# Optimization experiments

Hardware: AMD Instinct MI355X
Metric: run time of the kernel (lower is better)

The kernel has to match this reference:

```python
import math
import jax, jax.numpy as jnp
import numpy as np

B, S, D, H = 2, 4096, 512, 8
DH = D // H


def setup_inputs() -> dict:
    key = jax.random.key(0)
    ks = jax.random.split(key, 12)
    lim = 1.0 / math.sqrt(D)
    u = lambda k, shp: jax.random.uniform(k, shp, jnp.float32, -lim, lim)
    return {
        "x": jax.random.normal(ks[0], (B, S, D), jnp.float32),
        "gamma": jax.random.uniform(ks[1], (B, S, 1), jnp.float32),
        "Wq": u(ks[2], (D, D)), "bq": u(ks[3], (D,)),
        "Wk": u(ks[4], (D, D)), "bk": u(ks[5], (D,)),
        "Wv": u(ks[6], (D, D)), "bv": u(ks[7], (D,)),
        "Wo": u(ks[8], (D, D)), "bo": u(ks[9], (D,)),
    }


def reference(x, gamma, Wq, bq, Wk, bk, Wv, bv, Wo, bo):
    b, s, d = x.shape
    # projections (torch Linear: x @ W.T + b), split heads -> [B,H,S,DH]
    def proj(W, bias):
        return (x @ W.T + bias).reshape(b, s, H, DH).transpose(0, 2, 1, 3)
    q, k, v = proj(Wq, bq), proj(Wk, bk), proj(Wv, bv)

    scores = jnp.einsum("bhsd,bhtd->bhst", q, k) / math.sqrt(DH)  # [B,H,S,S]
    causal = jnp.triu(jnp.ones((s, s), bool), k=1)  # True above diagonal
    neg_inf = jnp.float32(-jnp.inf)
    scores = jnp.where(causal[None, None], neg_inf, scores)

    # hyperbolic positional bias: -log1p(gamma_i * max(i-j, 0) + 1e-8)
    pos = jnp.arange(s)
    delta = jnp.clip(pos[:, None] - pos[None, :], 0).astype(jnp.float32)  # [S,S]
    gamma_q = gamma[:, :, 0][:, :, None]  # [B,S,1]
    hyper = -jnp.log1p(gamma_q * delta + 1e-8)  # [B,S,S]
    hyper = jnp.where(causal[None], neg_inf, hyper)
    scores = scores + hyper[:, None]  # [B,H,S,S]

    attn = jax.nn.softmax(scores, axis=-1)
    out = jnp.einsum("bhst,bhtd->bhsd", attn, v)  # [B,H,S,DH]
    out = out.transpose(0, 2, 1, 3).reshape(b, s, d)
    return out @ Wo.T + bo
```

## Files before the change

kernel.cpp:

```cpp
#include <hip/hip_runtime.h>
#include <hip/hip_bf16.h>

#define Bb 2
#define Ss 4096
#define Dd 512
#define Hh 8
#define DHh 64

typedef __attribute__((ext_vector_type(8))) short short8;
typedef __attribute__((ext_vector_type(4))) float floatx4;

static __device__ __forceinline__ ushort bfbits(float f) {
  union { __hip_bfloat16 h; ushort u; } cv;
  cv.h = __float2bfloat16(f);
  return cv.u;
}

static __device__ __forceinline__ unsigned int packhi(float a, float b) {
  union { float f; unsigned int u; } ca, cb; ca.f = a; cb.f = b;
  return (ca.u >> 16) | (cb.u & 0xffff0000u);
}

__global__ void cvt_all(const float* __restrict__ x,
                        const float* __restrict__ w0, const float* __restrict__ w1,
                        const float* __restrict__ w2, const float* __restrict__ w3,
                        ushort* __restrict__ out) {
  const int XN4 = (Bb * Ss * Dd) / 4;
  const int WN4 = (Dd * Dd) / 4;
  int i = blockIdx.x * blockDim.x + threadIdx.x;
  if (i >= XN4 + 4 * WN4) return;
  const float* s; int li;
  if (i < XN4) { s = x; li = i; }
  else {
    int t = i - XN4; int j = t >> 16; li = t & (WN4 - 1);
    s = (j == 0) ? w0 : (j == 1) ? w1 : (j == 2) ? w2 : w3;
  }
  float4 f = ((const float4*)s)[li];
  ushort4 u;
  u.x = bfbits(f.x); u.y = bfbits(f.y); u.z = bfbits(f.z); u.w = bfbits(f.w);
  ((ushort4*)out)[i] = u;
}

static __device__ __forceinline__ int vperm(int s0) {
  int kb = (s0 >> 4) & 3, gq = (s0 >> 2) & 3;
  return (s0 & ~63) | ((kb >> 1) << 5) | (gq << 3) | ((kb & 1) << 2);
}

#define LDQK(buf, k0)                                                          \
  _Pragma("unroll")                                                            \
  for (int rb = 0; rb < 4; ++rb)                                               \
    af[buf][rb] = *(const short8*)(ap + (size_t)rb * 16 * 512 + (k0));         \
  _Pragma("unroll")                                                            \
  for (int cb = 0; cb < 4; ++cb)                                               \
    bf[buf][cb] = *(const short8*)(bp + (size_t)cb * 16 * 512 + (k0));

__global__ __launch_bounds__(256) void qkv_gemm(
    const ushort* __restrict__ xb,
    const ushort* __restrict__ Wq, const ushort* __restrict__ Wk, const ushort* __restrict__ Wv,
    const float* __restrict__ bq, const float* __restrict__ bk, const float* __restrict__ bv,
    ushort* __restrict__ qo, ushort* __restrict__ ko, ushort* __restrict__ vo)
{
  int mb = blockIdx.x / 12, rest = blockIdx.x % 12;
  int which = rest >> 2, nb = rest & 3;
  const ushort* Bw  = (which == 0) ? Wq : (which == 1) ? Wk : Wv;
  const float* bias = (which == 0) ? bq : (which == 1) ? bk : bv;
  int lane = threadIdx.x & 63, w = threadIdx.x >> 6;
  int wr = w & 1, wc = w >> 1;
  int g = lane >> 4, ln = lane & 15;
  int m0 = mb * 128 + wr * 64;
  int c0 = nb * 128 + wc * 64;
  const ushort* ap = xb + (size_t)(m0 + ln) * 512 + g * 8;
  const ushort* bp = Bw + (size_t)(c0 + ln) * 512 + g * 8;
  floatx4 acc[4][4] = {};
  short8 af[2][4], bf[2][4];
  LDQK(0, 0)
#pragma unroll
  for (int it = 0; it < 16; ++it) {
    int cur = it & 1;
    if (it < 15) { LDQK(cur ^ 1, (it + 1) * 32) }
#pragma unroll
    for (int rb = 0; rb < 4; ++rb)
#pragma unroll
      for (int cb = 0; cb < 4; ++cb)
        acc[rb][cb] = __builtin_amdgcn_mfma_f32_16x16x32_bf16(af[cur][rb], bf[cur][cb], acc[rb][cb], 0, 0, 0);
  }
  float scale = (which == 0) ? 0.18033688011112042f : 1.0f;
#pragma unroll
  for (int rb = 0; rb < 4; ++rb)
#pragma unroll
    for (int cb = 0; cb < 4; ++cb) {
      int col = c0 + cb * 16 + ln;
      float bv_ = bias[col];
      int hh = col >> 6, dh = col & 63;
      if (which == 2) {
        int i0 = m0 + rb * 16 + g * 4;
        int bI = i0 >> 12, s0 = i0 & (Ss - 1);
        ushort4 pk;
        pk.x = bfbits(acc[rb][cb][0] + bv_);
        pk.y = bfbits(acc[rb][cb][1] + bv_);
        pk.z = bfbits(acc[rb][cb][2] + bv_);
        pk.w = bfbits(acc[rb][cb][3] + bv_);
        *(ushort4*)(vo + (((size_t)bI * Hh + hh) * DHh + dh) * Ss + vperm(s0)) = pk;
      } else {
        ushort* outp = (which == 0) ? qo : ko;
#pragma unroll
        for (int r = 0; r < 4; ++r) {
          int i = m0 + rb * 16 + g * 4 + r;
          int bI = i >> 12, s = i & (Ss - 1);
          outp[(((size_t)bI * Hh + hh) * Ss + s) * DHh + dh] = bfbits((acc[rb][cb][r] + bv_) * scale);
        }
      }
    }
}

#define LD32(buf, k0)                                                          \
  af[buf][0] = *(const short8*)(ap + (k0));                                    \
  af[buf][1] = *(const short8*)(ap + 16 * 512 + (k0));                         \
  _Pragma("unroll")                                                            \
  for (int ns = 0; ns < 4; ++ns)                                               \
    bfr[buf][ns] = *(const short8*)(bp + (size_t)ns * 16 * 512 + (k0));

__global__ __launch_bounds__(256) void gemm_out(
    const ushort* __restrict__ A, const ushort* __restrict__ Bw,
    const float* __restrict__ bias, float* __restrict__ outp)
{
  int mb = blockIdx.x >> 3, nb = blockIdx.x & 7;
  int lane = threadIdx.x & 63, w = threadIdx.x >> 6;
  int g = lane >> 4, ln = lane & 15;
  int m0 = mb * 128 + w * 32;
  const ushort* ap = A + (size_t)(m0 + ln) * 512 + g * 8;
  const ushort* bp = Bw + (size_t)(nb * 64 + ln) * 512 + g * 8;
  floatx4 acc[2][4] = {};
  short8 af[2][2], bfr[2][4];
  LD32(0, 0)
#pragma unroll
  for (int it = 0; it < 16; ++it) {
    int cur = it & 1;
    if (it < 15) { LD32(cur ^ 1, (it + 1) * 32) }
#pragma unroll
    for (int ns = 0; ns < 4; ++ns) {
      acc[0][ns] = __builtin_amdgcn_mfma_f32_16x16x32_bf16(af[cur][0], bfr[cur][ns], acc[0][ns], 0, 0, 0);
      acc[1][ns] = __builtin_amdgcn_mfma_f32_16x16x32_bf16(af[cur][1], bfr[cur][ns], acc[1][ns], 0, 0, 0);
    }
  }
#pragma unroll
  for (int rb = 0; rb < 2; ++rb)
#pragma unroll
    for (int ns = 0; ns < 4; ++ns) {
      int col = nb * 64 + ns * 16 + ln;
      float bv_ = bias[col];
#pragma unroll
      for (int r = 0; r < 4; ++r)
        outp[(size_t)(m0 + rb * 16 + g * 4 + r) * 512 + col] = acc[rb][ns][r] + bv_;
    }
}

__global__ __launch_bounds__(128) void flash8(
    const ushort* __restrict__ q, const ushort* __restrict__ k,
    const ushort* __restrict__ vt, const float* __restrict__ gamma,
    ushort* __restrict__ o)
{
  __shared__ __align__(16) float Pmrg[64][34];
  __shared__ __align__(16) ushort Tb[16 * 72];

  int z = blockIdx.x;
  int bh = z & 15;
  int b = bh >> 3, hh = bh & 7;
  int sslot = (z >> 4) & 15, rnd = z >> 8;
  int j = (rnd << 4) | ((rnd & 1) ? (15 - sslot) : sslot);
  int u = j >> 1, qsel = j & 1;

  int tid = threadIdx.x;
  int half = tid >> 6, lane = tid & 63;
  int g = lane >> 4, ln = lane & 15;

  const ushort* kp = k + ((size_t)bh * Ss + ln) * DHh + g * 8;
  const ushort* vp = vt + ((size_t)bh * DHh + ln) * Ss + g * 8;

  int t = 2 * u + qsel;
  int q0 = t * 32;
  int ktm = u;
  int nkt = u + 1;
  int h = nkt >> 1;
  int lo = half ? h : 0, hi = half ? nkt : h;

  const ushort* qp = q + ((size_t)bh * Ss + q0 + ln) * DHh + g * 8;
  short8 qf00 = *(const short8*)qp;
  short8 qf01 = *(const short8*)(qp + 32);
  short8 qf10 = *(const short8*)(qp + 16 * DHh);
  short8 qf11 = *(const short8*)(qp + 16 * DHh + 32);

  int qrow0 = q0 + ln, qrow1 = q0 + 16 + ln;
  float gm0 = gamma[(size_t)b * Ss + qrow0];
  float gm1 = gamma[(size_t)b * Ss + qrow1];
  float l2[2] = {0.0f, 0.0f};
  floatx4 oacc[2][4] = {};

  short8 kfl[4], kfh[4], vf[8];
  int kb0 = lo * 64;
#pragma unroll
  for (int ns = 0; ns < 4; ++ns) {
    kfl[ns] = *(const short8*)(kp + (size_t)(kb0 + ns * 16) * DHh);
    kfh[ns] = *(const short8*)(kp + (size_t)(kb0 + ns * 16) * DHh + 32);
  }
#pragma unroll
  for (int cc = 0; cc < 8; ++cc)
    vf[cc] = *(const short8*)(vp + (size_t)((cc & 3) * 16) * Ss + kb0 + (cc >> 2) * 32);

  for (int kt = lo; kt < hi; ++kt) {
    int kbase = kt * 64;
    float sv[2][16];
#pragma unroll
    for (int ns = 0; ns < 4; ++ns) {
      floatx4 z0 = {}, z1 = {};
      z0 = __builtin_amdgcn_mfma_f32_16x16x32_bf16(kfl[ns], qf00, z0, 0, 0, 0);
      z0 = __builtin_amdgcn_mfma_f32_16x16x32_bf16(kfh[ns], qf01, z0, 0, 0, 0);
      z1 = __builtin_amdgcn_mfma_f32_16x16x32_bf16(kfl[ns], qf10, z1, 0, 0, 0);
      z1 = __builtin_amdgcn_mfma_f32_16x16x32_bf16(kfh[ns], qf11, z1, 0, 0, 0);
#pragma unroll
      for (int r = 0; r < 4; ++r) { sv[0][ns * 4 + r] = z0[r]; sv[1][ns * 4 + r] = z1[r]; }
    }
    if (kt + 1 < hi) {
      const ushort* kn = kp + (size_t)(kbase + 64) * DHh;
#pragma unroll
      for (int ns = 0; ns < 4; ++ns) {
        kfl[ns] = *(const short8*)(kn + (size_t)(ns * 16) * DHh);
        kfh[ns] = *(const short8*)(kn + (size_t)(ns * 16) * DHh + 32);
      }
    }
    bool last = (kt == ktm);
    short8 pfrag[2][2];
#pragma unroll
    for (int qb = 0; qb < 2; ++qb) {
      int qrow = qb ? qrow1 : qrow0;
      float gm = qb ? gm1 : gm0;
      int db = qrow - kbase - g * 4;
      float fd = (float)db;
      float rsub[4] = {0.0f, 0.0f, 0.0f, 0.0f};
      if (last) {
#pragma unroll
        for (int e = 0; e < 16; ++e) {
          int off = (e >> 2) * 16 + (e & 3);
          if (db - off < 0) sv[qb][e] = -1e30f;
          float delta = fmaxf(fd - (float)off, 0.0f);
          float wt = __builtin_amdgcn_rcpf(fmaf(gm, delta, 1.0f));
          float pv = __builtin_amdgcn_exp2f(sv[qb][e]) * wt;
          rsub[e & 3] += pv;
          sv[qb][e] = pv;
        }
      } else {
#pragma unroll
        for (int e = 0; e < 16; ++e) {
          float delta = fd - (float)((e >> 2) * 16 + (e & 3));
          float wt = __builtin_amdgcn_rcpf(fmaf(gm, delta, 1.0f));
          float pv = __builtin_amdgcn_exp2f(sv[qb][e]) * wt;
          rsub[e & 3] += pv;
          sv[qb][e] = pv;
        }
      }
      l2[qb] += (rsub[0] + rsub[1]) + (rsub[2] + rsub[3]);
#pragma unroll
      for (int c = 0; c < 2; ++c) {
        uint4 pkd;
        pkd.x = packhi(sv[qb][8 * c + 0], sv[qb][8 * c + 1]);
        pkd.y = packhi(sv[qb][8 * c + 2], sv[qb][8 * c + 3]);
        pkd.z = packhi(sv[qb][8 * c + 4], sv[qb][8 * c + 5]);
        pkd.w = packhi(sv[qb][8 * c + 6], sv[qb][8 * c + 7]);
        pfrag[qb][c] = *(short8*)&pkd;
      }
    }
#pragma unroll
    for (int c = 0; c < 2; ++c)
#pragma unroll
      for (int ds = 0; ds < 4; ++ds) {
        oacc[0][ds] = __builtin_amdgcn_mfma_f32_16x16x32_bf16(vf[c * 4 + ds], pfrag[0][c], oacc[0][ds], 0, 0, 0);
        oacc[1][ds] = __builtin_amdgcn_mfma_f32_16x16x32_bf16(vf[c * 4 + ds], pfrag[1][c], oacc[1][ds], 0, 0, 0);
      }
    if (kt + 1 < hi) {
#pragma unroll
      for (int cc = 0; cc < 8; ++cc)
        vf[cc] = *(const short8*)(vp + (size_t)((cc & 3) * 16) * Ss + kbase + 64 + (cc >> 2) * 32);
    }
  }

  if (half) {
#pragma unroll
    for (int qb = 0; qb < 2; ++qb)
#pragma unroll
      for (int ds = 0; ds < 4; ++ds)
#pragma unroll
        for (int r = 0; r < 4; ++r)
          Pmrg[lane][qb * 16 + ds * 4 + r] = oacc[qb][ds][r];
    Pmrg[lane][32] = l2[0];
    Pmrg[lane][33] = l2[1];
  }
  __syncthreads();
  if (!half) {
#pragma unroll
    for (int qb = 0; qb < 2; ++qb) {
#pragma unroll
      for (int ds = 0; ds < 4; ++ds)
#pragma unroll
        for (int r = 0; r < 4; ++r)
          oacc[qb][ds][r] += Pmrg[lane][qb * 16 + ds * 4 + r];
      float l = l2[qb] + Pmrg[lane][32 + qb];
      l += __shfl_xor(l, 16);
      l += __shfl_xor(l, 32);
      float linv = 1.0f / l;
      ushort* tb = &Tb[0];
#pragma unroll
      for (int ds = 0; ds < 4; ++ds)
#pragma unroll
        for (int r = 0; r < 4; ++r)
          tb[ln * 72 + ds * 16 + g * 4 + r] = bfbits(oacc[qb][ds][r] * linv);
      short8 v0 = *(const short8*)(tb + ln * 72 + g * 16);
      short8 v1 = *(const short8*)(tb + ln * 72 + g * 16 + 8);
      size_t oa = ((size_t)b * Ss + q0 + qb * 16 + ln) * Dd + hh * DHh + g * 16;
      *(short8*)(o + oa) = v0;
      *(short8*)(o + oa + 8) = v1;
    }
  }
}

extern "C" void kernel_launch(void* const* d_in, const int* in_sizes, int n_in,
                              void* d_out, int out_size, void* d_ws, size_t ws_size,
                              hipStream_t stream) {
  const float* x     = (const float*)d_in[0];
  const float* gamma = (const float*)d_in[1];
  const float* Wq    = (const float*)d_in[2];
  const float* bq    = (const float*)d_in[3];
  const float* Wk    = (const float*)d_in[4];
  const float* bk    = (const float*)d_in[5];
  const float* Wv    = (const float*)d_in[6];
  const float* bv    = (const float*)d_in[7];
  const float* Wo    = (const float*)d_in[8];
  const float* bo    = (const float*)d_in[9];

  const size_t NX = (size_t)Bb * Ss * Dd;
  const size_t NW = (size_t)Dd * Dd;
  ushort* xb  = (ushort*)d_ws;
  ushort* Wqb = xb + NX;
  ushort* Wkb = Wqb + NW;
  ushort* Wvb = Wkb + NW;
  ushort* Wob = Wvb + NW;
  ushort* qb  = Wob + NW;
  ushort* kb  = qb + NX;
  ushort* vtb = kb + NX;
  ushort* ab  = vtb + NX;

  const int total4 = (int)(NX / 4 + 4 * (NW / 4));
  cvt_all<<<(total4 + 255) / 256, 256, 0, stream>>>(x, Wq, Wk, Wv, Wo, xb);

  qkv_gemm<<<64 * 12, 256, 0, stream>>>(xb, Wqb, Wkb, Wvb, bq, bk, bv, qb, kb, vtb);

  flash8<<<2048, 128, 0, stream>>>(qb, kb, vtb, gamma, ab);

  gemm_out<<<512, 256, 0, stream>>>(ab, Wob, bo, (float*)d_out);
}
```

Baseline: 292.6 us.

## Pair complementary causal query tiles per block and split KV range over four waves

Replaces the 2-wave flash kernel with a 4-wave block that handles two query tiles, p and 63-p, so every block does the same total number of KV tiles. The 65 KV tiles are split evenly across the four waves, and partial outputs and row sums are combined with LDS atomicAdd into per-tile accumulators. This removes the load imbalance of the causal triangle and halves the grid. The cost is LDS atomic traffic, zero-initialisation of the accumulators, and an extra Q/gamma reload when a wave crosses the boundary between the two tiles.

New measurement: 305.6 us. +4.4%, slower.

```diff
diff --git a/kernel.cpp b/kernel.cpp
--- a/kernel.cpp
+++ b/kernel.cpp
@@ -155,164 +155,174 @@
     }
 }
 
-__global__ __launch_bounds__(128) void flash8(
+__global__ __launch_bounds__(256) void flash9(
     const ushort* __restrict__ q, const ushort* __restrict__ k,
     const ushort* __restrict__ vt, const float* __restrict__ gamma,
     ushort* __restrict__ o)
 {
-  __shared__ __align__(16) float Pmrg[64][34];
-  __shared__ __align__(16) ushort Tb[16 * 72];
+  __shared__ __align__(16) float Pacc[2][64][34];
+  __shared__ __align__(16) ushort Tb[2][16 * 72];
 
   int z = blockIdx.x;
   int bh = z & 15;
   int b = bh >> 3, hh = bh & 7;
-  int sslot = (z >> 4) & 15, rnd = z >> 8;
-  int j = (rnd << 4) | ((rnd & 1) ? (15 - sslot) : sslot);
-  int u = j >> 1, qsel = j & 1;
+  int qsel = (z >> 4) & 1;
+  int p = z >> 5;
+  int c = p + 1;
 
   int tid = threadIdx.x;
-  int half = tid >> 6, lane = tid & 63;
+  int wv = tid >> 6, lane = tid & 63;
   int g = lane >> 4, ln = lane & 15;
+
+  {
+    float* pz = &Pacc[0][0][0];
+#pragma unroll
+    for (int i = 0; i < 17; ++i) pz[tid + 256 * i] = 0.0f;
+  }
+  __syncthreads();
 
   const ushort* kp = k + ((size_t)bh * Ss + ln) * DHh + g * 8;
   const ushort* vp = vt + ((size_t)bh * DHh + ln) * Ss + g * 8;
 
-  int t = 2 * u + qsel;
-  int q0 = t * 32;
-  int ktm = u;
-  int nkt = u + 1;
-  int h = nkt >> 1;
-  int lo = half ? h : 0, hi = half ? nkt : h;
-
-  const ushort* qp = q + ((size_t)bh * Ss + q0 + ln) * DHh + g * 8;
-  short8 qf00 = *(const short8*)qp;
-  short8 qf01 = *(const short8*)(qp + 32);
-  short8 qf10 = *(const short8*)(qp + 16 * DHh);
-  short8 qf11 = *(const short8*)(qp + 16 * DHh + 32);
-
-  int qrow0 = q0 + ln, qrow1 = q0 + 16 + ln;
-  float gm0 = gamma[(size_t)b * Ss + qrow0];
-  float gm1 = gamma[(size_t)b * Ss + qrow1];
-  float l2[2] = {0.0f, 0.0f};
-  floatx4 oacc[2][4] = {};
-
-  short8 kfl[4], kfh[4], vf[8];
-  int kb0 = lo * 64;
-#pragma unroll
-  for (int ns = 0; ns < 4; ++ns) {
-    kfl[ns] = *(const short8*)(kp + (size_t)(kb0 + ns * 16) * DHh);
-    kfh[ns] = *(const short8*)(kp + (size_t)(kb0 + ns * 16) * DHh + 32);
-  }
-#pragma unroll
-  for (int cc = 0; cc < 8; ++cc)
-    vf[cc] = *(const short8*)(vp + (size_t)((cc & 3) * 16) * Ss + kb0 + (cc >> 2) * 32);
-
-  for (int kt = lo; kt < hi; ++kt) {
-    int kbase = kt * 64;
-    float sv[2][16];
+  int bw = 16 * wv + (wv > 0 ? 1 : 0);
+  int ew = 16 * (wv + 1) + 1;
+
+  for (int seg = 0; seg < 2; ++seg) {
+    int lo, hi, ut;
+    if (seg == 0) { lo = bw; hi = min(ew, c); ut = p; }
+    else { int s = max(bw, c); lo = s - c; hi = ew - c; ut = 63 - p; }
+    if (lo >= hi) continue;
+
+    int t = 2 * ut + qsel;
+    int q0 = t * 32;
+    int ktm = ut;
+
+    const ushort* qp = q + ((size_t)bh * Ss + q0 + ln) * DHh + g * 8;
+    short8 qf00 = *(const short8*)qp;
+    short8 qf01 = *(const short8*)(qp + 32);
+    short8 qf10 = *(const short8*)(qp + 16 * DHh);
+    short8 qf11 = *(const short8*)(qp + 16 * DHh + 32);
+
+    int qrow0 = q0 + ln, qrow1 = q0 + 16 + ln;
+    float gm0 = gamma[(size_t)b * Ss + qrow0];
+    float gm1 = gamma[(size_t)b * Ss + qrow1];
+    float l2[2] = {0.0f, 0.0f};
+    floatx4 oacc[2][4] = {};
+
+    short8 kfl[4], kfh[4], vf[8];
+    int kb0 = lo * 64;
 #pragma unroll
     for (int ns = 0; ns < 4; ++ns) {
-      floatx4 z0 = {}, z1 = {};
-      z0 = __builtin_amdgcn_mfma_f32_16x16x32_bf16(kfl[ns], qf00, z0, 0, 0, 0);
-      z0 = __builtin_amdgcn_mfma_f32_16x16x32_bf16(kfh[ns], qf01, z0, 0, 0, 0);
-      z1 = __builtin_amdgcn_mfma_f32_16x16x32_bf16(kfl[ns], qf10, z1, 0, 0, 0);
-      z1 = __builtin_amdgcn_mfma_f32_16x16x32_bf16(kfh[ns], qf11, z1, 0, 0, 0);
-#pragma unroll
-      for (int r = 0; r < 4; ++r) { sv[0][ns * 4 + r] = z0[r]; sv[1][ns * 4 + r] = z1[r]; }
-    }
-    if (kt + 1 < hi) {
-      const ushort* kn = kp + (size_t)(kbase + 64) * DHh;
+      kfl[ns] = *(const short8*)(kp + (size_t)(kb0 + ns * 16) * DHh);
+      kfh[ns] = *(const short8*)(kp + (size_t)(kb0 + ns * 16) * DHh + 32);
+    }
+#pragma unroll
+    for (int cc = 0; cc < 8; ++cc)
+      vf[cc] = *(const short8*)(vp + (size_t)((cc & 3) * 16) * Ss + kb0 + (cc >> 2) * 32);
+
+    for (int kt = lo; kt < hi; ++kt) {
+      int kbase = kt * 64;
+      float sv[2][16];
 #pragma unroll
       for (int ns = 0; ns < 4; ++ns) {
-        kfl[ns] = *(const short8*)(kn + (size_t)(ns * 16) * DHh);
-        kfh[ns] = *(const short8*)(kn + (size_t)(ns * 16) * DHh + 32);
-      }
-    }
-    bool last = (kt == ktm);
-    short8 pfrag[2][2];
+        floatx4 z0 = {}, z1 = {};
+        z0 = __builtin_amdgcn_mfma_f32_16x16x32_bf16(kfl[ns], qf00, z0, 0, 0, 0);
+        z0 = __builtin_amdgcn_mfma_f32_16x16x32_bf16(kfh[ns], qf01, z0, 0, 0, 0);
+        z1 = __builtin_amdgcn_mfma_f32_16x16x32_bf16(kfl[ns], qf10, z1, 0, 0, 0);
+        z1 = __builtin_amdgcn_mfma_f32_16x16x32_bf16(kfh[ns], qf11, z1, 0, 0, 0);
+#pragma unroll
+        for (int r = 0; r < 4; ++r) { sv[0][ns * 4 + r] = z0[r]; sv[1][ns * 4 + r] = z1[r]; }
+      }
+      if (kt + 1 < hi) {
+        const ushort* kn = kp + (size_t)(kbase + 64) * DHh;
+#pragma unroll
+        for (int ns = 0; ns < 4; ++ns) {
+          kfl[ns] = *(const short8*)(kn + (size_t)(ns * 16) * DHh);
+          kfh[ns] = *(const short8*)(kn + (size_t)(ns * 16) * DHh + 32);
+        }
+      }
+      bool last = (kt == ktm);
+      short8 pfrag[2][2];
+#pragma unroll
+      for (int qb = 0; qb < 2; ++qb) {
+        int qrow = qb ? qrow1 : qrow0;
+        float gm = qb ? gm1 : gm0;
+        int db = qrow - kbase - g * 4;
+        float fd = (float)db;
+        float rsub[4] = {0.0f, 0.0f, 0.0f, 0.0f};
+        if (last) {
+#pragma unroll
+          for (int e = 0; e < 16; ++e) {
+            int off = (e >> 2) * 16 + (e & 3);
+            if (db - off < 0) sv[qb][e] = -1e30f;
+            float delta = fmaxf(fd - (float)off, 0.0f);
+            float wt = __builtin_amdgcn_rcpf(fmaf(gm, delta, 1.0f));
+            float pv = __builtin_amdgcn_exp2f(sv[qb][e]) * wt;
+            rsub[e & 3] += pv;
+            sv[qb][e] = pv;
+          }
+        } else {
+#pragma unroll
+          for (int e = 0; e < 16; ++e) {
+            float delta = fd - (float)((e >> 2) * 16 + (e & 3));
+            float wt = __builtin_amdgcn_rcpf(fmaf(gm, delta, 1.0f));
+            float pv = __builtin_amdgcn_exp2f(sv[qb][e]) * wt;
+            rsub[e & 3] += pv;
+            sv[qb][e] = pv;
+          }
+        }
+        l2[qb] += (rsub[0] + rsub[1]) + (rsub[2] + rsub[3]);
+#pragma unroll
+        for (int cc = 0; cc < 2; ++cc) {
+          uint4 pkd;
+          pkd.x = packhi(sv[qb][8 * cc + 0], sv[qb][8 * cc + 1]);
+          pkd.y = packhi(sv[qb][8 * cc + 2], sv[qb][8 * cc + 3]);
+          pkd.z = packhi(sv[qb][8 * cc + 4], sv[qb][8 * cc + 5]);
+          pkd.w = packhi(sv[qb][8 * cc + 6], sv[qb][8 * cc + 7]);
+          pfrag[qb][cc] = *(short8*)&pkd;
+        }
+      }
+#pragma unroll
+      for (int cc = 0; cc < 2; ++cc)
+#pragma unroll
+        for (int ds = 0; ds < 4; ++ds) {
+          oacc[0][ds] = __builtin_amdgcn_mfma_f32_16x16x32_bf16(vf[cc * 4 + ds], pfrag[0][cc], oacc[0][ds], 0, 0, 0);
+          oacc[1][ds] = __builtin_amdgcn_mfma_f32_16x16x32_bf16(vf[cc * 4 + ds], pfrag[1][cc], oacc[1][ds], 0, 0, 0);
+        }
+      if (kt + 1 < hi) {
+#pragma unroll
+        for (int cc = 0; cc < 8; ++cc)
+          vf[cc] = *(const short8*)(vp + (size_t)((cc & 3) * 16) * Ss + kbase + 64 + (cc >> 2) * 32);
+      }
+    }
+
 #pragma unroll
     for (int qb = 0; qb < 2; ++qb) {
-      int qrow = qb ? qrow1 : qrow0;
-      float gm = qb ? gm1 : gm0;
-      int db = qrow - kbase - g * 4;
-      float fd = (float)db;
-      float rsub[4] = {0.0f, 0.0f, 0.0f, 0.0f};
-      if (last) {
-#pragma unroll
-        for (int e = 0; e < 16; ++e) {
-          int off = (e >> 2) * 16 + (e & 3);
-          if (db - off < 0) sv[qb][e] = -1e30f;
-          float delta = fmaxf(fd - (float)off, 0.0f);
-          float wt = __builtin_amdgcn_rcpf(fmaf(gm, delta, 1.0f));
-          float pv = __builtin_amdgcn_exp2f(sv[qb][e]) * wt;
-          rsub[e & 3] += pv;
-          sv[qb][e] = pv;
-        }
-      } else {
-#pragma unroll
-        for (int e = 0; e < 16; ++e) {
-          float delta = fd - (float)((e >> 2) * 16 + (e & 3));
-          float wt = __builtin_amdgcn_rcpf(fmaf(gm, delta, 1.0f));
-          float pv = __builtin_amdgcn_exp2f(sv[qb][e]) * wt;
-          rsub[e & 3] += pv;
-          sv[qb][e] = pv;
-        }
-      }
-      l2[qb] += (rsub[0] + rsub[1]) + (rsub[2] + rsub[3]);
-#pragma unroll
-      for (int c = 0; c < 2; ++c) {
-        uint4 pkd;
-        pkd.x = packhi(sv[qb][8 * c + 0], sv[qb][8 * c + 1]);
-        pkd.y = packhi(sv[qb][8 * c + 2], sv[qb][8 * c + 3]);
-        pkd.z = packhi(sv[qb][8 * c + 4], sv[qb][8 * c + 5]);
-        pkd.w = packhi(sv[qb][8 * c + 6], sv[qb][8 * c + 7]);
-        pfrag[qb][c] = *(short8*)&pkd;
-      }
-    }
-#pragma unroll
-    for (int c = 0; c < 2; ++c)
-#pragma unroll
-      for (int ds = 0; ds < 4; ++ds) {
-        oacc[0][ds] = __builtin_amdgcn_mfma_f32_16x16x32_bf16(vf[c * 4 + ds], pfrag[0][c], oacc[0][ds], 0, 0, 0);
-        oacc[1][ds] = __builtin_amdgcn_mfma_f32_16x16x32_bf16(vf[c * 4 + ds], pfrag[1][c], oacc[1][ds], 0, 0, 0);
-      }
-    if (kt + 1 < hi) {
-#pragma unroll
-      for (int cc = 0; cc < 8; ++cc)
-        vf[cc] = *(const short8*)(vp + (size_t)((cc & 3) * 16) * Ss + kbase + 64 + (cc >> 2) * 32);
-    }
-  }
-
-  if (half) {
-#pragma unroll
-    for (int qb = 0; qb < 2; ++qb)
 #pragma unroll
       for (int ds = 0; ds < 4; ++ds)
 #pragma unroll
         for (int r = 0; r < 4; ++r)
-          Pmrg[lane][qb * 16 + ds * 4 + r] = oacc[qb][ds][r];
-    Pmrg[lane][32] = l2[0];
-    Pmrg[lane][33] = l2[1];
-  }
+          atomicAdd(&Pacc[seg][lane][qb * 16 + ds * 4 + r], oacc[qb][ds][r]);
+      atomicAdd(&Pacc[seg][lane][32 + qb], l2[qb]);
+    }
+  }
+
   __syncthreads();
-  if (!half) {
+  if (wv < 2) {
+    int ut = wv ? (63 - p) : p;
+    int q0 = (2 * ut + qsel) * 32;
 #pragma unroll
     for (int qb = 0; qb < 2; ++qb) {
-#pragma unroll
-      for (int ds = 0; ds < 4; ++ds)
-#pragma unroll
-        for (int r = 0; r < 4; ++r)
-          oacc[qb][ds][r] += Pmrg[lane][qb * 16 + ds * 4 + r];
-      float l = l2[qb] + Pmrg[lane][32 + qb];
+      float l = Pacc[wv][lane][32 + qb];
       l += __shfl_xor(l, 16);
       l += __shfl_xor(l, 32);
       float linv = 1.0f / l;
-      ushort* tb = &Tb[0];
+      ushort* tb = &Tb[wv][0];
 #pragma unroll
       for (int ds = 0; ds < 4; ++ds)
 #pragma unroll
         for (int r = 0; r < 4; ++r)
-          tb[ln * 72 + ds * 16 + g * 4 + r] = bfbits(oacc[qb][ds][r] * linv);
+          tb[ln * 72 + ds * 16 + g * 4 + r] = bfbits(Pacc[wv][lane][qb * 16 + ds * 4 + r] * linv);
       short8 v0 = *(const short8*)(tb + ln * 72 + g * 16);
       short8 v1 = *(const short8*)(tb + ln * 72 + g * 16 + 8);
       size_t oa = ((size_t)b * Ss + q0 + qb * 16 + ln) * Dd + hh * DHh + g * 16;
@@ -353,7 +363,7 @@
 
   qkv_gemm<<<64 * 12, 256, 0, stream>>>(xb, Wqb, Wkb, Wvb, bq, bk, bv, qb, kb, vtb);
 
-  flash8<<<2048, 128, 0, stream>>>(qb, kb, vtb, gamma, ab);
+  flash9<<<1024, 256, 0, stream>>>(qb, kb, vtb, gamma, ab);
 
   gemm_out<<<512, 256, 0, stream>>>(ab, Wob, bo, (float*)d_out);
 }
```

## Pack both query tiles of a pair into one 256-thread flash block

Applied to the files above, without the earlier changes.

The flash kernel now runs both qsel query tiles sharing a key range in one 256-thread block (four waves: two query tiles times two key halves), halving the grid to 1024 blocks. Blocks are scheduled heaviest-first by counting u down from 63, replacing the interleaved serpentine ordering. The LDS merge buffers are doubled per query tile, and the non-last-tile weight computation hoists gamma*delta+1 into a per-row base. The aim is better co-scheduling and load balance, at the cost of tying each wave's lifetime to its sibling in the block and a launch-bounds occupancy hint of 3 that may constrain registers.

New measurement: 352.9 us. 20.6% more time.

```diff
diff --git a/kernel.cpp b/kernel.cpp
--- a/kernel.cpp
+++ b/kernel.cpp
@@ -155,23 +155,22 @@
     }
 }
 
-__global__ __launch_bounds__(128) void flash8(
+__global__ __launch_bounds__(256, 3) void flash11(
     const ushort* __restrict__ q, const ushort* __restrict__ k,
     const ushort* __restrict__ vt, const float* __restrict__ gamma,
     ushort* __restrict__ o)
 {
-  __shared__ __align__(16) float Pmrg[64][34];
-  __shared__ __align__(16) ushort Tb[16 * 72];
+  __shared__ __align__(16) float Pmrg[2][64][34];
+  __shared__ __align__(16) ushort Tb[2][16 * 72];
 
   int z = blockIdx.x;
   int bh = z & 15;
   int b = bh >> 3, hh = bh & 7;
-  int sslot = (z >> 4) & 15, rnd = z >> 8;
-  int j = (rnd << 4) | ((rnd & 1) ? (15 - sslot) : sslot);
-  int u = j >> 1, qsel = j & 1;
+  int u = 63 - (z >> 4);
 
   int tid = threadIdx.x;
-  int half = tid >> 6, lane = tid & 63;
+  int wv = tid >> 6, lane = tid & 63;
+  int qsel = wv >> 1, half = wv & 1;
   int g = lane >> 4, ln = lane & 15;
 
   const ushort* kp = k + ((size_t)bh * Ss + ln) * DHh + g * 8;
@@ -236,6 +235,7 @@
       float gm = qb ? gm1 : gm0;
       int db = qrow - kbase - g * 4;
       float fd = (float)db;
+      float base = fmaf(gm, fd, 1.0f);
       float rsub[4] = {0.0f, 0.0f, 0.0f, 0.0f};
       if (last) {
 #pragma unroll
@@ -251,8 +251,8 @@
       } else {
 #pragma unroll
         for (int e = 0; e < 16; ++e) {
-          float delta = fd - (float)((e >> 2) * 16 + (e & 3));
-          float wt = __builtin_amdgcn_rcpf(fmaf(gm, delta, 1.0f));
+          float off = (float)((e >> 2) * 16 + (e & 3));
+          float wt = __builtin_amdgcn_rcpf(fmaf(gm, -off, base));
           float pv = __builtin_amdgcn_exp2f(sv[qb][e]) * wt;
           rsub[e & 3] += pv;
           sv[qb][e] = pv;
@@ -260,21 +260,21 @@
       }
       l2[qb] += (rsub[0] + rsub[1]) + (rsub[2] + rsub[3]);
 #pragma unroll
-      for (int c = 0; c < 2; ++c) {
+      for (int cc = 0; cc < 2; ++cc) {
         uint4 pkd;
-        pkd.x = packhi(sv[qb][8 * c + 0], sv[qb][8 * c + 1]);
-        pkd.y = packhi(sv[qb][8 * c + 2], sv[qb][8 * c + 3]);
-        pkd.z = packhi(sv[qb][8 * c + 4], sv[qb][8 * c + 5]);
-        pkd.w = packhi(sv[qb][8 * c + 6], sv[qb][8 * c + 7]);
-        pfrag[qb][c] = *(short8*)&pkd;
-      }
-    }
-#pragma unroll
-    for (int c = 0; c < 2; ++c)
+        pkd.x = packhi(sv[qb][8 * cc + 0], sv[qb][8 * cc + 1]);
+        pkd.y = packhi(sv[qb][8 * cc + 2], sv[qb][8 * cc + 3]);
+        pkd.z = packhi(sv[qb][8 * cc + 4], sv[qb][8 * cc + 5]);
+        pkd.w = packhi(sv[qb][8 * cc + 6], sv[qb][8 * cc + 7]);
+        pfrag[qb][cc] = *(short8*)&pkd;
+      }
+    }
+#pragma unroll
+    for (int cc = 0; cc < 2; ++cc)
 #pragma unroll
       for (int ds = 0; ds < 4; ++ds) {
-        oacc[0][ds] = __builtin_amdgcn_mfma_f32_16x16x32_bf16(vf[c * 4 + ds], pfrag[0][c], oacc[0][ds], 0, 0, 0);
-        oacc[1][ds] = __builtin_amdgcn_mfma_f32_16x16x32_bf16(vf[c * 4 + ds], pfrag[1][c], oacc[1][ds], 0, 0, 0);
+        oacc[0][ds] = __builtin_amdgcn_mfma_f32_16x16x32_bf16(vf[cc * 4 + ds], pfrag[0][cc], oacc[0][ds], 0, 0, 0);
+        oacc[1][ds] = __builtin_amdgcn_mfma_f32_16x16x32_bf16(vf[cc * 4 + ds], pfrag[1][cc], oacc[1][ds], 0, 0, 0);
       }
     if (kt + 1 < hi) {
 #pragma unroll
@@ -290,9 +290,9 @@
       for (int ds = 0; ds < 4; ++ds)
 #pragma unroll
         for (int r = 0; r < 4; ++r)
-          Pmrg[lane][qb * 16 + ds * 4 + r] = oacc[qb][ds][r];
-    Pmrg[lane][32] = l2[0];
-    Pmrg[lane][33] = l2[1];
+          Pmrg[qsel][lane][qb * 16 + ds * 4 + r] = oacc[qb][ds][r];
+    Pmrg[qsel][lane][32] = l2[0];
+    Pmrg[qsel][lane][33] = l2[1];
   }
   __syncthreads();
   if (!half) {
@@ -302,12 +302,12 @@
       for (int ds = 0; ds < 4; ++ds)
 #pragma unroll
         for (int r = 0; r < 4; ++r)
-          oacc[qb][ds][r] += Pmrg[lane][qb * 16 + ds * 4 + r];
-      float l = l2[qb] + Pmrg[lane][32 + qb];
+          oacc[qb][ds][r] += Pmrg[qsel][lane][qb * 16 + ds * 4 + r];
+      float l = l2[qb] + Pmrg[qsel][lane][32 + qb];
       l += __shfl_xor(l, 16);
       l += __shfl_xor(l, 32);
       float linv = 1.0f / l;
-      ushort* tb = &Tb[0];
+      ushort* tb = &Tb[qsel][0];
 #pragma unroll
       for (int ds = 0; ds < 4; ++ds)
 #pragma unroll
@@ -353,7 +353,7 @@
 
   qkv_gemm<<<64 * 12, 256, 0, stream>>>(xb, Wqb, Wkb, Wvb, bq, bk, bv, qb, kb, vtb);
 
-  flash8<<<2048, 128, 0, stream>>>(qb, kb, vtb, gamma, ab);
+  flash11<<<1024, 256, 0, stream>>>(qb, kb, vtb, gamma, ab);
 
   gemm_out<<<512, 256, 0, stream>>>(ab, Wob, bo, (float*)d_out);
 }
```
